# Kernel optimization log

Measured on AMD Instinct MI355X. Metric: run time of the kernel, lower is better.

The kernel has to match this reference:

```python
import jax, jax.numpy as jnp
import numpy as np
import math

B, T, D = 2, 2048, 1024
H, HS = 16, 64  # n_heads, head_size; D == H*HS


def setup_inputs() -> dict:
    key = jax.random.key(0)
    k1, k2, k3 = jax.random.split(key, 3)
    x = jax.random.normal(k1, (B, T, D), dtype=jnp.float32)
    w_qkv = jax.random.normal(k2, (D, 3 * D), dtype=jnp.float32) * (1.0 / math.sqrt(D))
    b_qkv = jnp.zeros((3 * D,), dtype=jnp.float32)
    w_out = jax.random.normal(k3, (D, D), dtype=jnp.float32) * (1.0 / math.sqrt(D))
    b_out = jnp.zeros((D,), dtype=jnp.float32)
    return {"x": x, "w_qkv": w_qkv, "b_qkv": b_qkv, "w_out": w_out, "b_out": b_out}


def reference(x, w_qkv, b_qkv, w_out, b_out):
    b, t, d = x.shape
    qkv = x @ w_qkv + b_qkv                       # (B,T,3D)
    q, k, v = jnp.split(qkv, 3, axis=-1)
    # (B,T,D) -> (B,H,T,HS)
    q = q.reshape(b, t, H, HS).transpose(0, 2, 1, 3)
    k = k.reshape(b, t, H, HS).transpose(0, 2, 1, 3)
    v = v.reshape(b, t, H, HS).transpose(0, 2, 1, 3)
    scale = 1.0 / math.sqrt(HS)
    attn = jnp.einsum('bhqd,bhkd->bhqk', q, k) * scale  # (B,H,T,T)
    causal = jnp.tril(jnp.ones((t, t), dtype=bool))
    attn = jnp.where(causal[None, None], attn, -jnp.inf)
    attn = jax.nn.softmax(attn, axis=-1)
    o = jnp.einsum('bhqk,bhkd->bhqd', attn, v)          # (B,H,T,HS)
    o = o.transpose(0, 2, 1, 3).reshape(b, t, d)
    return o @ w_out + b_out
```

## Files before the change

kernel.cpp:

```cpp
#include <hip/hip_runtime.h>
#include <math.h>

#define B_  2
#define T_  2048
#define D_  1024
#define H_  16
#define HS_ 64
#define M_  (B_*T_)

typedef __bf16 bf16x8 __attribute__((ext_vector_type(8)));
typedef float  f32x4  __attribute__((ext_vector_type(4)));
typedef unsigned short u16;

static __device__ __forceinline__ u16 f2bf(float f) {
    __bf16 h = (__bf16)f;
    return *reinterpret_cast<u16*>(&h);
}

static __device__ __forceinline__ void glds16(const u16* g, u16* l) {
    __builtin_amdgcn_global_load_lds(
        (const __attribute__((address_space(1))) void*)g,
        (__attribute__((address_space(3))) void*)l, 16, 0, 0);
}

__global__ __launch_bounds__(256) void prep_kernel(
    const float* __restrict__ x, const float* __restrict__ w_qkv,
    const float* __restrict__ w_out,
    u16* __restrict__ Xb, u16* __restrict__ WqkvT, u16* __restrict__ WoutT)
{
    int bid = blockIdx.x;
    if (bid < 4096) {
        int i = (bid * 256 + threadIdx.x) * 4;
        float4 v = *reinterpret_cast<const float4*>(x + i);
        ushort4 o;
        o.x = f2bf(v.x); o.y = f2bf(v.y); o.z = f2bf(v.z); o.w = f2bf(v.w);
        *reinterpret_cast<ushort4*>(Xb + i) = o;
        return;
    }
    const float* in; u16* out; int C; int c0, r0;
    if (bid < 4096 + 3072) {
        int t = bid - 4096;
        in = w_qkv; out = WqkvT; C = 3 * D_;
        c0 = (t % 96) * 32; r0 = (t / 96) * 32;
    } else {
        int t = bid - 7168;
        in = w_out; out = WoutT; C = D_;
        c0 = (t & 31) * 32; r0 = (t >> 5) * 32;
    }
    __shared__ float tile[32][33];
    int tr = threadIdx.x >> 3, tc4 = (threadIdx.x & 7) * 4;
    float4 v = *reinterpret_cast<const float4*>(in + (size_t)(r0 + tr) * C + c0 + tc4);
    tile[tr][tc4+0] = v.x; tile[tr][tc4+1] = v.y;
    tile[tr][tc4+2] = v.z; tile[tr][tc4+3] = v.w;
    __syncthreads();
    ushort4 o;
    o.x = f2bf(tile[tc4+0][tr]); o.y = f2bf(tile[tc4+1][tr]);
    o.z = f2bf(tile[tc4+2][tr]); o.w = f2bf(tile[tc4+3][tr]);
    *reinterpret_cast<ushort4*>(out + (size_t)(c0 + tr) * D_ + r0 + tc4) = o;
}

__global__ __launch_bounds__(512, 2) void gemm_qkv(
    const u16* __restrict__ A, const u16* __restrict__ Bt,
    const float* __restrict__ bias,
    u16* __restrict__ Qb, u16* __restrict__ Kb, u16* __restrict__ Vt)
{
    constexpr int K  = D_;
    constexpr int NT = K / 64;

    __shared__ u16 LDS[2][2][2][8192];

    const int tid  = threadIdx.x;
    const int lane = tid & 63, wave = tid >> 6;
    const int wm = wave >> 2, wn = wave & 3;
    const int quad = lane >> 4, lr = lane & 15;
    const int bm = blockIdx.x, bn = blockIdx.y;

    const u16* Ab = A  + (size_t)(bm * 256) * K;
    const u16* Bb = Bt + (size_t)(bn * 256) * K;

    const int r0 = tid >> 2;
    const int c0 = (tid & 3) ^ ((tid >> 3) & 3);
    const u16* sA0 = Ab + (size_t)r0 * K + c0 * 8;
    const u16* sA1 = sA0 + (size_t)128 * K;
    const u16* sB0 = Bb + (size_t)r0 * K + c0 * 8;
    const u16* sB1 = sB0 + (size_t)128 * K;
    const int d0 = tid * 8, d1 = (tid + 512) * 8;

    const int swz = (lr >> 1) & 3;
    const int eA = ((wm*128 + lr) * 4 + (quad ^ swz)) * 8;
    const int eB = ((wn*64  + lr) * 4 + (quad ^ swz)) * 8;

    f32x4 acc[8][4] = {};

#define STG(mat, kh, tt) do { \
        u16* _d = &LDS[(tt) & 1][mat][kh][0]; \
        const int _ko = (tt) * 64 + (kh) * 32; \
        glds16(((mat) ? sB0 : sA0) + _ko, _d + d0); \
        glds16(((mat) ? sB1 : sA1) + _ko, _d + d1); \
    } while (0)

#define MFMA_QUAD(mh) do { \
        __builtin_amdgcn_s_setprio(1); \
        _Pragma("unroll") \
        for (int i_ = 0; i_ < 4; ++i_) \
            _Pragma("unroll") \
            for (int j_ = 0; j_ < 4; ++j_) \
                acc[(mh)*4 + i_][j_] = __builtin_amdgcn_mfma_f32_16x16x32_bf16( \
                    a[i_], b[j_], acc[(mh)*4 + i_][j_], 0, 0, 0); \
        __builtin_amdgcn_s_setprio(0); \
    } while (0)

    STG(0,0,0); STG(1,0,0); STG(0,1,0); STG(1,1,0);
    asm volatile("s_waitcnt vmcnt(4)" ::: "memory");
    __builtin_amdgcn_s_barrier();

    for (int t = 0; t < NT; ++t) {
        const int cb = t & 1;
        const bool last = (t == NT - 1);
        const u16* Ar0 = &LDS[cb][0][0][0];
        const u16* Ar1 = &LDS[cb][0][1][0];
        const u16* Br0 = &LDS[cb][1][0][0];
        const u16* Br1 = &LDS[cb][1][1][0];
        bf16x8 a[4], b[4];

        #pragma unroll
        for (int i = 0; i < 4; ++i) a[i] = *reinterpret_cast<const bf16x8*>(Ar0 + eA + i*512);
        #pragma unroll
        for (int j = 0; j < 4; ++j) b[j] = *reinterpret_cast<const bf16x8*>(Br0 + eB + j*512);
        if (!last) STG(0,0,t+1);
        __builtin_amdgcn_s_barrier();
        asm volatile("s_waitcnt lgkmcnt(0)" ::: "memory");
        MFMA_QUAD(0);
        __builtin_amdgcn_s_barrier();

        #pragma unroll
        for (int i = 0; i < 4; ++i) a[i] = *reinterpret_cast<const bf16x8*>(Ar0 + eA + (i+4)*512);
        if (!last) STG(1,0,t+1);
        __builtin_amdgcn_s_barrier();
        asm volatile("s_waitcnt lgkmcnt(0)" ::: "memory");
        MFMA_QUAD(1);
        if (!last) { asm volatile("s_waitcnt vmcnt(4)" ::: "memory"); }
        else       { asm volatile("s_waitcnt vmcnt(0)" ::: "memory"); }
        __builtin_amdgcn_s_barrier();

        #pragma unroll
        for (int i = 0; i < 4; ++i) a[i] = *reinterpret_cast<const bf16x8*>(Ar1 + eA + i*512);
        #pragma unroll
        for (int j = 0; j < 4; ++j) b[j] = *reinterpret_cast<const bf16x8*>(Br1 + eB + j*512);
        if (!last) STG(0,1,t+1);
        __builtin_amdgcn_s_barrier();
        asm volatile("s_waitcnt lgkmcnt(0)" ::: "memory");
        MFMA_QUAD(0);
        __builtin_amdgcn_s_barrier();

        #pragma unroll
        for (int i = 0; i < 4; ++i) a[i] = *reinterpret_cast<const bf16x8*>(Ar1 + eA + (i+4)*512);
        if (!last) STG(1,1,t+1);
        __builtin_amdgcn_s_barrier();
        asm volatile("s_waitcnt lgkmcnt(0)" ::: "memory");
        MFMA_QUAD(1);
        asm volatile("s_waitcnt vmcnt(4)" ::: "memory");
        __builtin_amdgcn_s_barrier();
    }
#undef STG
#undef MFMA_QUAD

    #pragma unroll
    for (int i = 0; i < 8; ++i) {
        int m0 = bm*256 + wm*128 + i*16 + quad*4;
        #pragma unroll
        for (int j = 0; j < 4; ++j) {
            int ncol = bn*256 + wn*64 + j*16 + lr;
            float bv = bias[ncol];
            float v4[4];
            #pragma unroll
            for (int r = 0; r < 4; ++r) v4[r] = acc[i][j][r] + bv;
            int bb = m0 >> 11, t0 = m0 & (T_ - 1);
            int s = ncol >> 10, rem = ncol & 1023;
            int h = rem >> 6, d = rem & 63;
            int bh = bb * H_ + h;
            if (s == 0) {
                #pragma unroll
                for (int r = 0; r < 4; ++r)
                    Qb[((size_t)bh*T_ + t0 + r)*HS_ + d] = f2bf(v4[r] * 0.1803368801111244f);
            } else if (s == 1) {
                #pragma unroll
                for (int r = 0; r < 4; ++r)
                    Kb[((size_t)bh*T_ + t0 + r)*HS_ + d] = f2bf(v4[r]);
            } else {
                ushort4 o;
                o.x = f2bf(v4[0]); o.y = f2bf(v4[1]);
                o.z = f2bf(v4[2]); o.w = f2bf(v4[3]);
                *reinterpret_cast<ushort4*>(&Vt[((size_t)bh*HS_ + d)*T_ + t0]) = o;
            }
        }
    }
}

__global__ __launch_bounds__(256, 2) void gemm_out(
    const u16* __restrict__ A, const u16* __restrict__ Bt,
    const float* __restrict__ bias, float* __restrict__ Cf)
{
    constexpr int K  = D_;
    constexpr int N  = D_;
    constexpr int NT = K / 64;

    __shared__ u16 LDS[2][2][2][4096];

    const int tid  = threadIdx.x;
    const int lane = tid & 63, wave = tid >> 6;
    const int wm = wave >> 1, wn = wave & 1;
    const int quad = lane >> 4, lr = lane & 15;
    const int bm = blockIdx.x, bn = blockIdx.y;

    const u16* Ab = A  + (size_t)(bm * 128) * K;
    const u16* Bb = Bt + (size_t)(bn * 128) * K;

    const int r0 = tid >> 2;
    const int c0 = (tid & 3) ^ ((tid >> 3) & 3);
    const u16* sA0 = Ab + (size_t)r0 * K + c0 * 8;
    const u16* sA1 = sA0 + (size_t)64 * K;
    const u16* sB0 = Bb + (size_t)r0 * K + c0 * 8;
    const u16* sB1 = sB0 + (size_t)64 * K;
    const int d0 = tid * 8, d1 = (tid + 256) * 8;

    const int swz = (lr >> 1) & 3;
    const int eA = ((wm*64 + lr) * 4 + (quad ^ swz)) * 8;
    const int eB = ((wn*64 + lr) * 4 + (quad ^ swz)) * 8;

    f32x4 acc[4][4] = {};

#define STGO(kh, tt) do { \
        const int _ko = (tt) * 64 + (kh) * 32; \
        glds16(sA0 + _ko, &LDS[(tt) & 1][0][kh][0] + d0); \
        glds16(sA1 + _ko, &LDS[(tt) & 1][0][kh][0] + d1); \
        glds16(sB0 + _ko, &LDS[(tt) & 1][1][kh][0] + d0); \
        glds16(sB1 + _ko, &LDS[(tt) & 1][1][kh][0] + d1); \
    } while (0)

    STGO(0, 0); STGO(1, 0);
    asm volatile("s_waitcnt vmcnt(4)" ::: "memory");
    __builtin_amdgcn_s_barrier();

    for (int t = 0; t < NT; ++t) {
        const int cb = t & 1;
        const bool last = (t == NT - 1);
        bf16x8 a[4], b[4];

        {
            const u16* Ar = &LDS[cb][0][0][0];
            const u16* Br = &LDS[cb][1][0][0];
            #pragma unroll
            for (int i = 0; i < 4; ++i) a[i] = *reinterpret_cast<const bf16x8*>(Ar + eA + i*512);
            #pragma unroll
            for (int j = 0; j < 4; ++j) b[j] = *reinterpret_cast<const bf16x8*>(Br + eB + j*512);
            if (!last) STGO(0, t+1);
            __builtin_amdgcn_s_barrier();
            asm volatile("s_waitcnt lgkmcnt(0)" ::: "memory");
            __builtin_amdgcn_s_setprio(1);
            #pragma unroll
            for (int i = 0; i < 4; ++i)
                #pragma unroll
                for (int j = 0; j < 4; ++j)
                    acc[i][j] = __builtin_amdgcn_mfma_f32_16x16x32_bf16(a[i], b[j], acc[i][j], 0, 0, 0);
            __builtin_amdgcn_s_setprio(0);
            if (!last) { asm volatile("s_waitcnt vmcnt(4)" ::: "memory"); }
            else       { asm volatile("s_waitcnt vmcnt(0)" ::: "memory"); }
            __builtin_amdgcn_s_barrier();
        }

        {
            const u16* Ar = &LDS[cb][0][1][0];
            const u16* Br = &LDS[cb][1][1][0];
            #pragma unroll
            for (int i = 0; i < 4; ++i) a[i] = *reinterpret_cast<const bf16x8*>(Ar + eA + i*512);
            #pragma unroll
            for (int j = 0; j < 4; ++j) b[j] = *reinterpret_cast<const bf16x8*>(Br + eB + j*512);
            if (!last) STGO(1, t+1);
            __builtin_amdgcn_s_barrier();
            asm volatile("s_waitcnt lgkmcnt(0)" ::: "memory");
            __builtin_amdgcn_s_setprio(1);
            #pragma unroll
            for (int i = 0; i < 4; ++i)
                #pragma unroll
                for (int j = 0; j < 4; ++j)
                    acc[i][j] = __builtin_amdgcn_mfma_f32_16x16x32_bf16(a[i], b[j], acc[i][j], 0, 0, 0);
            __builtin_amdgcn_s_setprio(0);
            if (!last) { asm volatile("s_waitcnt vmcnt(4)" ::: "memory"); }
            __builtin_amdgcn_s_barrier();
        }
    }
#undef STGO

    #pragma unroll
    for (int i = 0; i < 4; ++i) {
        int m0 = bm*128 + wm*64 + i*16 + quad*4;
        #pragma unroll
        for (int j = 0; j < 4; ++j) {
            int ncol = bn*128 + wn*64 + j*16 + lr;
            float bv = bias[ncol];
            #pragma unroll
            for (int r = 0; r < 4; ++r)
                Cf[(size_t)(m0 + r) * N + ncol] = acc[i][j][r] + bv;
        }
    }
}

__global__ __launch_bounds__(256) void attn_kernel(
    const u16* __restrict__ Qb, const u16* __restrict__ Kb,
    const u16* __restrict__ Vt, u16* __restrict__ Ob)
{
    __shared__ u16 Ks[64 * 64];
    __shared__ u16 Vs[64 * 64];
    __shared__ u16 Ps[4][16 * 64];

    int tid  = threadIdx.x;
    int lane = tid & 63, wave = tid >> 6;
    int quad = lane >> 4, lr = lane & 15;

    int lin = blockIdx.x;
    int bh  = (lin & 7) + 8 * ((lin >> 3) & 3);
    int idx = lin >> 5;
    int qt  = idx < 16 ? idx : 47 - idx;
    int qw  = qt * 64 + wave * 16;

    const u16* Qp = Qb + ((size_t)bh * T_ + qw) * HS_;
    bf16x8 qf[2];
    #pragma unroll
    for (int h2 = 0; h2 < 2; ++h2)
        qf[h2] = *reinterpret_cast<const bf16x8*>(Qp + lr*HS_ + h2*32 + quad*8);

    f32x4 Oa[4] = {};
    float lrow[4] = {0.f, 0.f, 0.f, 0.f};

    int e      = quad ^ (lr & 7);
    int rb0    = (lr * 8 + e) * 8;
    int rb1    = (lr * 8 + (e ^ 4)) * 8;
    int offw[4][4];
    #pragma unroll
    for (int nt = 0; nt < 4; ++nt)
        #pragma unroll
        for (int r = 0; r < 4; ++r) {
            int prow = quad*4 + r;
            offw[nt][r] = (prow*8 + ((nt*2 + (lr >> 3)) ^ (prow & 7)))*8 + (lr & 7);
        }
    u16* Psw = Ps[wave];

    int srow = tid >> 3;
    int scol = ((tid & 7) ^ (srow & 7)) * 8;
    const u16* kp0 = Kb + ((size_t)bh*T_ + srow     )*HS_ + scol;
    const u16* kp1 = Kb + ((size_t)bh*T_ + srow + 32)*HS_ + scol;
    const u16* vp0 = Vt + ((size_t)bh*HS_ + srow     )*T_ + scol;
    const u16* vp1 = Vt + ((size_t)bh*HS_ + srow + 32)*T_ + scol;

    bf16x8 kpre0 = *reinterpret_cast<const bf16x8*>(kp0);
    bf16x8 kpre1 = *reinterpret_cast<const bf16x8*>(kp1);
    bf16x8 vpre0 = *reinterpret_cast<const bf16x8*>(vp0);
    bf16x8 vpre1 = *reinterpret_cast<const bf16x8*>(vp1);

    for (int jt = 0; jt <= qt; ++jt) {
        __syncthreads();
        reinterpret_cast<bf16x8*>(Ks)[tid]       = kpre0;
        reinterpret_cast<bf16x8*>(Ks)[tid + 256] = kpre1;
        reinterpret_cast<bf16x8*>(Vs)[tid]       = vpre0;
        reinterpret_cast<bf16x8*>(Vs)[tid + 256] = vpre1;
        if (jt < qt) {
            kp0 += 64*HS_; kp1 += 64*HS_; vp0 += 64; vp1 += 64;
            kpre0 = *reinterpret_cast<const bf16x8*>(kp0);
            kpre1 = *reinterpret_cast<const bf16x8*>(kp1);
            vpre0 = *reinterpret_cast<const bf16x8*>(vp0);
            vpre1 = *reinterpret_cast<const bf16x8*>(vp1);
        }
        __syncthreads();

        f32x4 Sa[4] = {};
        #pragma unroll
        for (int nt = 0; nt < 4; ++nt) {
            bf16x8 bk0 = *reinterpret_cast<const bf16x8*>(Ks + rb0 + nt*1024);
            bf16x8 bk1 = *reinterpret_cast<const bf16x8*>(Ks + rb1 + nt*1024);
            Sa[nt] = __builtin_amdgcn_mfma_f32_16x16x32_bf16(qf[0], bk0, Sa[nt], 0, 0, 0);
            Sa[nt] = __builtin_amdgcn_mfma_f32_16x16x32_bf16(qf[1], bk1, Sa[nt], 0, 0, 0);
        }

        if (jt == qt) {
            int kb = jt * 64;
            #pragma unroll
            for (int nt = 0; nt < 4; ++nt)
                #pragma unroll
                for (int r = 0; r < 4; ++r) {
                    int kg = kb + nt*16 + lr;
                    int qg = qw + quad*4 + r;
                    if (kg > qg) Sa[nt][r] = -INFINITY;
                }
        }

        #pragma unroll
        for (int nt = 0; nt < 4; ++nt)
            #pragma unroll
            for (int r = 0; r < 4; ++r) {
                float pv = __builtin_amdgcn_exp2f(Sa[nt][r]);
                lrow[r] += pv;
                Psw[offw[nt][r]] = f2bf(pv);
            }

        #pragma unroll
        for (int kk = 0; kk < 2; ++kk) {
            int rb = kk ? rb1 : rb0;
            bf16x8 pa = *reinterpret_cast<const bf16x8*>(Psw + rb);
            #pragma unroll
            for (int nt = 0; nt < 4; ++nt) {
                bf16x8 vb = *reinterpret_cast<const bf16x8*>(Vs + rb + nt*1024);
                Oa[nt] = __builtin_amdgcn_mfma_f32_16x16x32_bf16(pa, vb, Oa[nt], 0, 0, 0);
            }
        }
    }

    int b = bh >> 4, h = bh & 15;
    #pragma unroll
    for (int r = 0; r < 4; ++r) {
        float s = lrow[r];
        #pragma unroll
        for (int off = 8; off >= 1; off >>= 1)
            s += __shfl_xor(s, off, 64);
        float inv = 1.f / s;
        int qg = qw + quad*4 + r;
        #pragma unroll
        for (int nt = 0; nt < 4; ++nt) {
            int d = nt*16 + lr;
            Ob[((size_t)b*T_ + qg)*D_ + h*HS_ + d] = f2bf(Oa[nt][r] * inv);
        }
    }
}

extern "C" void kernel_launch(void* const* d_in, const int* in_sizes, int n_in,
                              void* d_out, int out_size, void* d_ws, size_t ws_size,
                              hipStream_t stream) {
    (void)in_sizes; (void)n_in; (void)out_size; (void)ws_size;
    const float* x     = (const float*)d_in[0];
    const float* w_qkv = (const float*)d_in[1];
    const float* b_qkv = (const float*)d_in[2];
    const float* w_out = (const float*)d_in[3];
    const float* b_out = (const float*)d_in[4];
    float* out = (float*)d_out;

    char* ws = (char*)d_ws;
    u16* Xb    = (u16*)ws; ws += (size_t)M_ * D_ * 2;
    u16* WqkvT = (u16*)ws; ws += (size_t)3 * D_ * D_ * 2;
    u16* WoutT = (u16*)ws; ws += (size_t)D_ * D_ * 2;
    u16* Qb    = (u16*)ws; ws += (size_t)M_ * D_ * 2;
    u16* Kb    = (u16*)ws; ws += (size_t)M_ * D_ * 2;
    u16* Vt    = (u16*)ws; ws += (size_t)M_ * D_ * 2;
    u16* Ob    = (u16*)ws; ws += (size_t)M_ * D_ * 2;

    prep_kernel<<<8192, 256, 0, stream>>>(x, w_qkv, w_out, Xb, WqkvT, WoutT);
    gemm_qkv<<<dim3(M_/256, 3*D_/256), 512, 0, stream>>>(
        Xb, WqkvT, b_qkv, Qb, Kb, Vt);
    attn_kernel<<<1024, 256, 0, stream>>>(Qb, Kb, Vt, Ob);
    gemm_out<<<dim3(M_/128, D_/128), 256, 0, stream>>>(Ob, WoutT, b_out, out);
}
```

Before: 171.7 us.

## Pair low/high causal query tiles per attention block and remap QKV GEMM blocks to XCDs

Each attention block now handles two query tiles, p and 31-p, so every block does the same amount of causal work. Each K/V tile loaded into LDS is reused for both query tiles, which halves the grid and cuts redundant K/V loads. MFMA sections are wrapped in s_setprio. The QKV GEMM grid index is remapped so blocks scheduled on the same XCD share A/B panels in cache. The cost is more registers per thread for the doubled accumulators and fewer blocks, which may reduce occupancy.

```diff
diff --git a/kernel.cpp b/kernel.cpp
--- a/kernel.cpp
+++ b/kernel.cpp
@@ -73,7 +73,11 @@
     const int lane = tid & 63, wave = tid >> 6;
     const int wm = wave >> 2, wn = wave & 3;
     const int quad = lane >> 4, lr = lane & 15;
-    const int bm = blockIdx.x, bn = blockIdx.y;
+
+    const int lin = blockIdx.x + 16 * blockIdx.y;
+    const int xcd = lin & 7, rr = lin >> 3;
+    const int bm = (xcd & 3) * 4 + (rr & 3);
+    const int bn = (xcd >> 2) * 6 + (rr >> 2);
 
     const u16* Ab = A  + (size_t)(bm * 256) * K;
     const u16* Bb = Bt + (size_t)(bn * 256) * K;
@@ -312,7 +316,7 @@
 {
     __shared__ u16 Ks[64 * 64];
     __shared__ u16 Vs[64 * 64];
-    __shared__ u16 Ps[4][16 * 64];
+    __shared__ u16 Ps[4][2][16 * 64];
 
     int tid  = threadIdx.x;
     int lane = tid & 63, wave = tid >> 6;
@@ -320,22 +324,26 @@
 
     int lin = blockIdx.x;
     int bh  = (lin & 7) + 8 * ((lin >> 3) & 3);
-    int idx = lin >> 5;
-    int qt  = idx < 16 ? idx : 47 - idx;
-    int qw  = qt * 64 + wave * 16;
-
-    const u16* Qp = Qb + ((size_t)bh * T_ + qw) * HS_;
-    bf16x8 qf[2];
+    int p   = lin >> 5;
+    int qlo = p, qhi = 31 - p;
+    int rlo = qlo * 64 + wave * 16;
+    int rhi = qhi * 64 + wave * 16;
+
+    const u16* QpL = Qb + ((size_t)bh * T_ + rlo) * HS_;
+    const u16* QpH = Qb + ((size_t)bh * T_ + rhi) * HS_;
+    bf16x8 qfL[2], qfH[2];
     #pragma unroll
-    for (int h2 = 0; h2 < 2; ++h2)
-        qf[h2] = *reinterpret_cast<const bf16x8*>(Qp + lr*HS_ + h2*32 + quad*8);
-
-    f32x4 Oa[4] = {};
-    float lrow[4] = {0.f, 0.f, 0.f, 0.f};
-
-    int e      = quad ^ (lr & 7);
-    int rb0    = (lr * 8 + e) * 8;
-    int rb1    = (lr * 8 + (e ^ 4)) * 8;
+    for (int h2 = 0; h2 < 2; ++h2) {
+        qfL[h2] = *reinterpret_cast<const bf16x8*>(QpL + lr*HS_ + h2*32 + quad*8);
+        qfH[h2] = *reinterpret_cast<const bf16x8*>(QpH + lr*HS_ + h2*32 + quad*8);
+    }
+
+    f32x4 OaL[4] = {}, OaH[4] = {};
+    float lrL[4] = {0.f,0.f,0.f,0.f}, lrH[4] = {0.f,0.f,0.f,0.f};
+
+    int e   = quad ^ (lr & 7);
+    int rb0 = (lr * 8 + e) * 8;
+    int rb1 = (lr * 8 + (e ^ 4)) * 8;
     int offw[4][4];
     #pragma unroll
     for (int nt = 0; nt < 4; ++nt)
@@ -344,7 +352,8 @@
             int prow = quad*4 + r;
             offw[nt][r] = (prow*8 + ((nt*2 + (lr >> 3)) ^ (prow & 7)))*8 + (lr & 7);
         }
-    u16* Psw = Ps[wave];
+    u16* PsL = Ps[wave][0];
+    u16* PsH = Ps[wave][1];
 
     int srow = tid >> 3;
     int scol = ((tid & 7) ^ (srow & 7)) * 8;
@@ -358,13 +367,13 @@
     bf16x8 vpre0 = *reinterpret_cast<const bf16x8*>(vp0);
     bf16x8 vpre1 = *reinterpret_cast<const bf16x8*>(vp1);
 
-    for (int jt = 0; jt <= qt; ++jt) {
+    for (int jt = 0; jt <= qhi; ++jt) {
         __syncthreads();
         reinterpret_cast<bf16x8*>(Ks)[tid]       = kpre0;
         reinterpret_cast<bf16x8*>(Ks)[tid + 256] = kpre1;
         reinterpret_cast<bf16x8*>(Vs)[tid]       = vpre0;
         reinterpret_cast<bf16x8*>(Vs)[tid + 256] = vpre1;
-        if (jt < qt) {
+        if (jt < qhi) {
             kp0 += 64*HS_; kp1 += 64*HS_; vp0 += 64; vp1 += 64;
             kpre0 = *reinterpret_cast<const bf16x8*>(kp0);
             kpre1 = *reinterpret_cast<const bf16x8*>(kp1);
@@ -373,61 +382,113 @@
         }
         __syncthreads();
 
-        f32x4 Sa[4] = {};
+        const bool lo = (jt <= qlo);
+
+        f32x4 SaH[4] = {}, SaL[4] = {};
+        __builtin_amdgcn_s_setprio(1);
         #pragma unroll
         for (int nt = 0; nt < 4; ++nt) {
             bf16x8 bk0 = *reinterpret_cast<const bf16x8*>(Ks + rb0 + nt*1024);
             bf16x8 bk1 = *reinterpret_cast<const bf16x8*>(Ks + rb1 + nt*1024);
-            Sa[nt] = __builtin_amdgcn_mfma_f32_16x16x32_bf16(qf[0], bk0, Sa[nt], 0, 0, 0);
-            Sa[nt] = __builtin_amdgcn_mfma_f32_16x16x32_bf16(qf[1], bk1, Sa[nt], 0, 0, 0);
-        }
-
-        if (jt == qt) {
+            SaH[nt] = __builtin_amdgcn_mfma_f32_16x16x32_bf16(qfH[0], bk0, SaH[nt], 0, 0, 0);
+            SaH[nt] = __builtin_amdgcn_mfma_f32_16x16x32_bf16(qfH[1], bk1, SaH[nt], 0, 0, 0);
+        }
+        if (lo) {
+            #pragma unroll
+            for (int nt = 0; nt < 4; ++nt) {
+                bf16x8 bk0 = *reinterpret_cast<const bf16x8*>(Ks + rb0 + nt*1024);
+                bf16x8 bk1 = *reinterpret_cast<const bf16x8*>(Ks + rb1 + nt*1024);
+                SaL[nt] = __builtin_amdgcn_mfma_f32_16x16x32_bf16(qfL[0], bk0, SaL[nt], 0, 0, 0);
+                SaL[nt] = __builtin_amdgcn_mfma_f32_16x16x32_bf16(qfL[1], bk1, SaL[nt], 0, 0, 0);
+            }
+        }
+        __builtin_amdgcn_s_setprio(0);
+
+        if (jt == qhi) {
             int kb = jt * 64;
             #pragma unroll
             for (int nt = 0; nt < 4; ++nt)
                 #pragma unroll
                 for (int r = 0; r < 4; ++r) {
                     int kg = kb + nt*16 + lr;
-                    int qg = qw + quad*4 + r;
-                    if (kg > qg) Sa[nt][r] = -INFINITY;
+                    int qg = rhi + quad*4 + r;
+                    if (kg > qg) SaH[nt][r] = -INFINITY;
                 }
         }
+        if (jt == qlo) {
+            int kb = jt * 64;
+            #pragma unroll
+            for (int nt = 0; nt < 4; ++nt)
+                #pragma unroll
+                for (int r = 0; r < 4; ++r) {
+                    int kg = kb + nt*16 + lr;
+                    int qg = rlo + quad*4 + r;
+                    if (kg > qg) SaL[nt][r] = -INFINITY;
+                }
+        }
 
         #pragma unroll
         for (int nt = 0; nt < 4; ++nt)
             #pragma unroll
             for (int r = 0; r < 4; ++r) {
-                float pv = __builtin_amdgcn_exp2f(Sa[nt][r]);
-                lrow[r] += pv;
-                Psw[offw[nt][r]] = f2bf(pv);
+                float pv = __builtin_amdgcn_exp2f(SaH[nt][r]);
+                lrH[r] += pv;
+                PsH[offw[nt][r]] = f2bf(pv);
             }
-
+        if (lo) {
+            #pragma unroll
+            for (int nt = 0; nt < 4; ++nt)
+                #pragma unroll
+                for (int r = 0; r < 4; ++r) {
+                    float pv = __builtin_amdgcn_exp2f(SaL[nt][r]);
+                    lrL[r] += pv;
+                    PsL[offw[nt][r]] = f2bf(pv);
+                }
+        }
+
+        __builtin_amdgcn_s_setprio(1);
         #pragma unroll
         for (int kk = 0; kk < 2; ++kk) {
             int rb = kk ? rb1 : rb0;
-            bf16x8 pa = *reinterpret_cast<const bf16x8*>(Psw + rb);
+            bf16x8 pa = *reinterpret_cast<const bf16x8*>(PsH + rb);
             #pragma unroll
             for (int nt = 0; nt < 4; ++nt) {
                 bf16x8 vb = *reinterpret_cast<const bf16x8*>(Vs + rb + nt*1024);
-                Oa[nt] = __builtin_amdgcn_mfma_f32_16x16x32_bf16(pa, vb, Oa[nt], 0, 0, 0);
+                OaH[nt] = __builtin_amdgcn_mfma_f32_16x16x32_bf16(pa, vb, OaH[nt], 0, 0, 0);
             }
         }
+        if (lo) {
+            #pragma unroll
+            for (int kk = 0; kk < 2; ++kk) {
+                int rb = kk ? rb1 : rb0;
+                bf16x8 pa = *reinterpret_cast<const bf16x8*>(PsL + rb);
+                #pragma unroll
+                for (int nt = 0; nt < 4; ++nt) {
+                    bf16x8 vb = *reinterpret_cast<const bf16x8*>(Vs + rb + nt*1024);
+                    OaL[nt] = __builtin_amdgcn_mfma_f32_16x16x32_bf16(pa, vb, OaL[nt], 0, 0, 0);
+                }
+            }
+        }
+        __builtin_amdgcn_s_setprio(0);
     }
 
     int b = bh >> 4, h = bh & 15;
     #pragma unroll
     for (int r = 0; r < 4; ++r) {
-        float s = lrow[r];
-        #pragma unroll
-        for (int off = 8; off >= 1; off >>= 1)
-            s += __shfl_xor(s, off, 64);
-        float inv = 1.f / s;
-        int qg = qw + quad*4 + r;
+        float sH = lrH[r], sL = lrL[r];
+        #pragma unroll
+        for (int off = 8; off >= 1; off >>= 1) {
+            sH += __shfl_xor(sH, off, 64);
+            sL += __shfl_xor(sL, off, 64);
+        }
+        float invH = 1.f / sH, invL = 1.f / sL;
+        int qgH = rhi + quad*4 + r;
+        int qgL = rlo + quad*4 + r;
         #pragma unroll
         for (int nt = 0; nt < 4; ++nt) {
             int d = nt*16 + lr;
-            Ob[((size_t)b*T_ + qg)*D_ + h*HS_ + d] = f2bf(Oa[nt][r] * inv);
+            Ob[((size_t)b*T_ + qgH)*D_ + h*HS_ + d] = f2bf(OaH[nt][r] * invH);
+            Ob[((size_t)b*T_ + qgL)*D_ + h*HS_ + d] = f2bf(OaL[nt][r] * invL);
         }
     }
 }
@@ -453,8 +514,8 @@
     u16* Ob    = (u16*)ws; ws += (size_t)M_ * D_ * 2;
 
     prep_kernel<<<8192, 256, 0, stream>>>(x, w_qkv, w_out, Xb, WqkvT, WoutT);
-    gemm_qkv<<<dim3(M_/256, 3*D_/256), 512, 0, stream>>>(
+    gemm_qkv<<<dim3(16, 12), 512, 0, stream>>>(
         Xb, WqkvT, b_qkv, Qb, Kb, Vt);
-    attn_kernel<<<1024, 256, 0, stream>>>(Qb, Kb, Vt, Ob);
+    attn_kernel<<<512, 256, 0, stream>>>(Qb, Kb, Vt, Ob);
     gemm_out<<<dim3(M_/128, D_/128), 256, 0, stream>>>(Ob, WoutT, b_out, out);
 }
```

Measured after the change: 175.9 us. 2.5% more time.
